# Optimization experiments

Measured on AMD Instinct MI355X. Metric: run time of the kernel, lower is better.

The kernel has to match this reference:

```python
import jax, jax.numpy as jnp
import numpy as np

B, IN_DIM, HID, ATT = 16384, 128, 512, 256
TOTAL = IN_DIM + HID + ATT


def setup_inputs() -> dict:
    key = jax.random.key(0)
    ks = jax.random.split(key, 10)
    u = lambda k, shape, lo, hi: jax.random.uniform(k, shape, jnp.float32, lo, hi)
    return {
        "t": jnp.float32(0.0),
        "h_ltc": jax.random.normal(ks[0], (B, HID), jnp.float32),
        "x_t": jax.random.normal(ks[1], (B, IN_DIM), jnp.float32),
        "context": jax.random.normal(ks[2], (B, ATT), jnp.float32),
        "W_gd": u(ks[3], (2 * HID, TOTAL), -0.1, 0.1),
        "b_gd": u(ks[4], (2 * HID,), -0.1, 0.1),
        "W_tau": u(ks[5], (HID, HID), -0.1, 0.1),
        "b_tau": u(ks[6], (HID,), -0.1, 0.1),
        "gleak": u(ks[7], (HID,), 0.001, 1.0),
        "cm": u(ks[8], (HID,), 0.4, 0.6),
    }


def reference(t, h_ltc, x_t, context, W_gd, b_gd, W_tau, b_tau, gleak, cm):
    # combined: [B, IN+HID+ATT]
    combined = jnp.concatenate([x_t, h_ltc, context], axis=1)
    g_d = combined @ W_gd.T + b_gd            # [B, 2*HID]
    gate, dynamics = jnp.split(g_d, 2, axis=1)
    tau = jax.nn.softplus(h_ltc @ W_tau.T + b_tau)  # [B, HID]
    numerator = jax.nn.sigmoid(gate) * jnp.tanh(dynamics) - h_ltc
    denominator = tau + jax.nn.softplus(cm) + jax.nn.softplus(gleak)
    return numerator / (denominator + 1e-6)
```

## Files before the change

### kernel.cpp

```cpp
#include <hip/hip_runtime.h>
#include <hip/hip_bf16.h>
#include <math.h>

#define BROWS 16384
#define IN_DIM 128
#define HID 512
#define ATT 256
#define KTOT 896
#define KC_TOT 112

typedef __bf16 bf16x8 __attribute__((ext_vector_type(8)));
typedef float f32x4 __attribute__((ext_vector_type(4)));

__device__ __forceinline__ float softplus_f(float x) {
    return fmaxf(x, 0.0f) + log1pf(__expf(-fabsf(x)));
}

__global__ void pack_B(const float* __restrict__ W_gd, const float* __restrict__ W_tau,
                       const float* __restrict__ gleak, const float* __restrict__ cm,
                       __hip_bfloat16* __restrict__ B_stage, float* __restrict__ dconst) {
    const int cid = blockIdx.x * 256 + threadIdx.x;
    if (cid < HID) {
        dconst[cid] = softplus_f(cm[cid]) + softplus_f(gleak[cid]) + 1e-6f;
    }
    const int nl = cid % 192;
    const int kc = (cid / 192) % KC_TOT;
    const int jt = cid / (192 * KC_TOT);
    const int jg = nl / 48, type = (nl % 48) / 16, j16 = nl % 16;
    const int j = jt * 64 + jg * 16 + j16;
    const int k0 = kc * 8;

    float v[8];
    if (type == 0) {
        const float* s = W_gd + (size_t)j * KTOT + k0;
        #pragma unroll
        for (int i = 0; i < 8; ++i) v[i] = s[i];
    } else if (type == 1) {
        const float* s = W_gd + (size_t)(HID + j) * KTOT + k0;
        #pragma unroll
        for (int i = 0; i < 8; ++i) v[i] = s[i];
    } else {
        if (k0 >= IN_DIM && k0 < IN_DIM + HID) {
            const float* s = W_tau + (size_t)j * HID + (k0 - IN_DIM);
            #pragma unroll
            for (int i = 0; i < 8; ++i) v[i] = s[i];
        } else {
            #pragma unroll
            for (int i = 0; i < 8; ++i) v[i] = 0.0f;
        }
    }
    union { __hip_bfloat16 hh[8]; uint4 u; } p;
    #pragma unroll
    for (int i = 0; i < 8; ++i) p.hh[i] = __float2bfloat16(v[i]);
    *(uint4*)(B_stage + (size_t)cid * 8) = p.u;
}

__global__ __launch_bounds__(512, 2) void ltc_gemm(
    const float* __restrict__ x, const float* __restrict__ h_ltc,
    const float* __restrict__ ctx, const __hip_bfloat16* __restrict__ B_stage,
    const float* __restrict__ b_gd, const float* __restrict__ b_tau,
    const float* __restrict__ dconst, float* __restrict__ out) {

    __shared__ __attribute__((aligned(16))) char As[57344];

    const int mt = blockIdx.x;
    const int tid = threadIdx.x;
    const int wave = tid >> 6, lane = tid & 63;
    const int q = lane >> 4, t = lane & 15;

    const int mi = tid >> 4;
    const int kcg = tid & 15;
    #pragma unroll
    for (int s = 0; s < 7; ++s) {
        const int kc = kcg + 16 * s;
        const float* src; int rs, col;
        if (s == 0)      { src = x;     rs = IN_DIM; col = kcg * 8; }
        else if (s < 5)  { src = h_ltc; rs = HID;    col = kcg * 8 + (s - 1) * 128; }
        else             { src = ctx;   rs = ATT;    col = kcg * 8 + (s - 5) * 128; }
        const float* p = src + (size_t)(mt * 32 + mi) * rs + col;
        float4 v0 = *(const float4*)p;
        float4 v1 = *(const float4*)(p + 4);
        union { __hip_bfloat16 hh[8]; uint4 u; } pk;
        pk.hh[0] = __float2bfloat16(v0.x); pk.hh[1] = __float2bfloat16(v0.y);
        pk.hh[2] = __float2bfloat16(v0.z); pk.hh[3] = __float2bfloat16(v0.w);
        pk.hh[4] = __float2bfloat16(v1.x); pk.hh[5] = __float2bfloat16(v1.y);
        pk.hh[6] = __float2bfloat16(v1.z); pk.hh[7] = __float2bfloat16(v1.w);
        *(uint4*)(As + ((kc * 32 + (mi ^ (kc & 31))) << 4)) = pk.u;
    }
    __syncthreads();

    for (int it = 0; it < 4; ++it) {
        const int jglob = it * 128 + wave * 16;
        const int jt = jglob >> 6;
        const int jg = (jglob >> 4) & 3;
        const __hip_bfloat16* bBase = B_stage
            + ((size_t)jt * (KC_TOT * 192) + jg * 48 + t) * 8;

        f32x4 acc[2][3];
        #pragma unroll
        for (int f = 0; f < 2; ++f)
            #pragma unroll
            for (int ty = 0; ty < 3; ++ty) acc[f][ty] = (f32x4)0.0f;

        bf16x8 ab[4][2]; bf16x8 bb[4][3];

        #pragma unroll
        for (int p = 0; p < 2; ++p) {
            const int kc = p * 4 + q;
            const int sw = kc & 31;
            ab[p][0] = *(const bf16x8*)(As + ((kc * 32 + (t ^ sw)) << 4));
            ab[p][1] = *(const bf16x8*)(As + ((kc * 32 + ((16 + t) ^ sw)) << 4));
        }
        #pragma unroll
        for (int p = 0; p < 3; ++p) {
            const __hip_bfloat16* bp = bBase + (size_t)(p * 4 + q) * 1536;
            bb[p][0] = *(const bf16x8*)(bp);
            bb[p][1] = *(const bf16x8*)(bp + 128);
        }

        #pragma unroll 4
        for (int kst = 0; kst < 28; ++kst) {
            const int ca = kst & 3;
            if (kst < 26) {
                const int kc = (kst + 2) * 4 + q;
                const int sw = kc & 31;
                const int na = (kst + 2) & 3;
                ab[na][0] = *(const bf16x8*)(As + ((kc * 32 + (t ^ sw)) << 4));
                ab[na][1] = *(const bf16x8*)(As + ((kc * 32 + ((16 + t) ^ sw)) << 4));
            }
            if (kst < 25) {
                const int kc = (kst + 3) * 4 + q;
                const int nbf = (kst + 3) & 3;
                const __hip_bfloat16* bp = bBase + (size_t)kc * 1536;
                bb[nbf][0] = *(const bf16x8*)(bp);
                bb[nbf][1] = *(const bf16x8*)(bp + 128);
                if (kst + 3 >= 4 && kst + 3 < 20)
                    bb[nbf][2] = *(const bf16x8*)(bp + 256);
            }
            const bool tau_cur = (kst >= 4 && kst < 20);
            acc[0][0] = __builtin_amdgcn_mfma_f32_16x16x32_bf16(ab[ca][0], bb[ca][0], acc[0][0], 0, 0, 0);
            acc[1][0] = __builtin_amdgcn_mfma_f32_16x16x32_bf16(ab[ca][1], bb[ca][0], acc[1][0], 0, 0, 0);
            acc[0][1] = __builtin_amdgcn_mfma_f32_16x16x32_bf16(ab[ca][0], bb[ca][1], acc[0][1], 0, 0, 0);
            acc[1][1] = __builtin_amdgcn_mfma_f32_16x16x32_bf16(ab[ca][1], bb[ca][1], acc[1][1], 0, 0, 0);
            if (tau_cur) {
                acc[0][2] = __builtin_amdgcn_mfma_f32_16x16x32_bf16(ab[ca][0], bb[ca][2], acc[0][2], 0, 0, 0);
                acc[1][2] = __builtin_amdgcn_mfma_f32_16x16x32_bf16(ab[ca][1], bb[ca][2], acc[1][2], 0, 0, 0);
            }
        }

        const int j = jglob + t;
        const float bgj = b_gd[j];
        const float bdj = b_gd[HID + j];
        const float btj = b_tau[j];
        const float dcj = dconst[j];
        #pragma unroll
        for (int f = 0; f < 2; ++f) {
            #pragma unroll
            for (int r = 0; r < 4; ++r) {
                const int row = mt * 32 + f * 16 + q * 4 + r;
                const float gv = acc[f][0][r] + bgj;
                const float dv = acc[f][1][r] + bdj;
                const float tp = acc[f][2][r] + btj;
                const float hv = h_ltc[(size_t)row * HID + j];
                const float sig = __builtin_amdgcn_rcpf(1.0f + __expf(-gv));
                const float th  = 1.0f - 2.0f * __builtin_amdgcn_rcpf(__expf(2.0f * dv) + 1.0f);
                const float tau = fmaxf(tp, 0.0f) + __logf(1.0f + __expf(-fabsf(tp)));
                out[(size_t)row * HID + j] = (sig * th - hv) * __builtin_amdgcn_rcpf(tau + dcj);
            }
        }
    }
}

extern "C" void kernel_launch(void* const* d_in, const int* in_sizes, int n_in,
                              void* d_out, int out_size, void* d_ws, size_t ws_size,
                              hipStream_t stream) {
    const float* h_ltc = (const float*)d_in[1];
    const float* x_t   = (const float*)d_in[2];
    const float* ctx   = (const float*)d_in[3];
    const float* W_gd  = (const float*)d_in[4];
    const float* b_gd  = (const float*)d_in[5];
    const float* W_tau = (const float*)d_in[6];
    const float* b_tau = (const float*)d_in[7];
    const float* gleak = (const float*)d_in[8];
    const float* cm    = (const float*)d_in[9];

    char* ws = (char*)d_ws;
    __hip_bfloat16* B_stage = (__hip_bfloat16*)ws;
    float* dconst = (float*)(ws + 2752512);

    pack_B<<<672, 256, 0, stream>>>(W_gd, W_tau, gleak, cm, B_stage, dconst);
    ltc_gemm<<<512, 512, 0, stream>>>(x_t, h_ltc, ctx, B_stage, b_gd, b_tau, dconst,
                                      (float*)d_out);
}
```

Baseline: 179.8 us.

## Restructure GEMM into 64x256 tiles with double-buffered LDS B staging

Each workgroup now computes a 64-row by 256-column output tile instead of 32 rows across all 512 columns. The weight tile is staged into LDS with asynchronous global-to-LDS loads and the activations are streamed per K-step, both double-buffered. Block indices are remapped so tiles sharing rows land on the same XCD. The aim is to replace per-wave global B reads with LDS reuse and to overlap loading with MFMA work, at the cost of a larger register accumulator set (24 f32x4) and a barrier every K-step.

```diff
diff --git a/kernel.cpp b/kernel.cpp
--- a/kernel.cpp
+++ b/kernel.cpp
@@ -55,112 +55,143 @@
     *(uint4*)(B_stage + (size_t)cid * 8) = p.u;
 }
 
+#define LDSB 49152
+#define LDSBUF 53248
+
 __global__ __launch_bounds__(512, 2) void ltc_gemm(
     const float* __restrict__ x, const float* __restrict__ h_ltc,
     const float* __restrict__ ctx, const __hip_bfloat16* __restrict__ B_stage,
     const float* __restrict__ b_gd, const float* __restrict__ b_tau,
     const float* __restrict__ dconst, float* __restrict__ out) {
 
-    __shared__ __attribute__((aligned(16))) char As[57344];
-
-    const int mt = blockIdx.x;
+    __shared__ __attribute__((aligned(16))) char Lds[2][LDSBUF];
+
+    const int wgid = blockIdx.x;
+    const int xcd = wgid & 7;
+    const int k2 = wgid >> 3;
+    const int jt2 = k2 & 1;
+    const int rt = xcd * 32 + (k2 >> 1);
+    const int jtBase = jt2 * 4;
+
     const int tid = threadIdx.x;
     const int wave = tid >> 6, lane = tid & 63;
     const int q = lane >> 4, t = lane & 15;
 
-    const int mi = tid >> 4;
-    const int kcg = tid & 15;
-    #pragma unroll
-    for (int s = 0; s < 7; ++s) {
-        const int kc = kcg + 16 * s;
-        const float* src; int rs, col;
-        if (s == 0)      { src = x;     rs = IN_DIM; col = kcg * 8; }
-        else if (s < 5)  { src = h_ltc; rs = HID;    col = kcg * 8 + (s - 1) * 128; }
-        else             { src = ctx;   rs = ATT;    col = kcg * 8 + (s - 5) * 128; }
-        const float* p = src + (size_t)(mt * 32 + mi) * rs + col;
+    int bo[6];
+    #pragma unroll
+    for (int i = 0; i < 6; ++i) {
+        const int n = i * 512 + tid;
+        const int kcl = n / 768;
+        const int jtl = (n / 192) & 3;
+        const int nl  = n - (n / 192) * 192;
+        bo[i] = (((jtBase + jtl) * KC_TOT + kcl) * 192 + nl) * 16;
+    }
+    const char* bsrc = (const char*)B_stage;
+
+    const int arow = (tid & 255) >> 2;
+    const int ach  = tid & 3;
+
+    #pragma unroll
+    for (int i = 0; i < 6; ++i) {
+        const int n = i * 512 + tid;
+        __builtin_amdgcn_global_load_lds(
+            (const __attribute__((address_space(1))) void*)(bsrc + bo[i]),
+            (__attribute__((address_space(3))) void*)(&Lds[0][n * 16]), 16, 0, 0);
+    }
+    if (tid < 256) {
+        const float* p = x + (size_t)(rt * 64 + arow) * IN_DIM + ach * 8;
         float4 v0 = *(const float4*)p;
         float4 v1 = *(const float4*)(p + 4);
         union { __hip_bfloat16 hh[8]; uint4 u; } pk;
-        pk.hh[0] = __float2bfloat16(v0.x); pk.hh[1] = __float2bfloat16(v0.y);
-        pk.hh[2] = __float2bfloat16(v0.z); pk.hh[3] = __float2bfloat16(v0.w);
-        pk.hh[4] = __float2bfloat16(v1.x); pk.hh[5] = __float2bfloat16(v1.y);
-        pk.hh[6] = __float2bfloat16(v1.z); pk.hh[7] = __float2bfloat16(v1.w);
-        *(uint4*)(As + ((kc * 32 + (mi ^ (kc & 31))) << 4)) = pk.u;
-    }
-    __syncthreads();
-
-    for (int it = 0; it < 4; ++it) {
-        const int jglob = it * 128 + wave * 16;
-        const int jt = jglob >> 6;
-        const int jg = (jglob >> 4) & 3;
-        const __hip_bfloat16* bBase = B_stage
-            + ((size_t)jt * (KC_TOT * 192) + jg * 48 + t) * 8;
-
-        f32x4 acc[2][3];
-        #pragma unroll
-        for (int f = 0; f < 2; ++f)
-            #pragma unroll
-            for (int ty = 0; ty < 3; ++ty) acc[f][ty] = (f32x4)0.0f;
-
-        bf16x8 ab[4][2]; bf16x8 bb[4][3];
-
-        #pragma unroll
-        for (int p = 0; p < 2; ++p) {
-            const int kc = p * 4 + q;
-            const int sw = kc & 31;
-            ab[p][0] = *(const bf16x8*)(As + ((kc * 32 + (t ^ sw)) << 4));
-            ab[p][1] = *(const bf16x8*)(As + ((kc * 32 + ((16 + t) ^ sw)) << 4));
-        }
-        #pragma unroll
-        for (int p = 0; p < 3; ++p) {
-            const __hip_bfloat16* bp = bBase + (size_t)(p * 4 + q) * 1536;
-            bb[p][0] = *(const bf16x8*)(bp);
-            bb[p][1] = *(const bf16x8*)(bp + 128);
-        }
-
-        #pragma unroll 4
-        for (int kst = 0; kst < 28; ++kst) {
-            const int ca = kst & 3;
-            if (kst < 26) {
-                const int kc = (kst + 2) * 4 + q;
-                const int sw = kc & 31;
-                const int na = (kst + 2) & 3;
-                ab[na][0] = *(const bf16x8*)(As + ((kc * 32 + (t ^ sw)) << 4));
-                ab[na][1] = *(const bf16x8*)(As + ((kc * 32 + ((16 + t) ^ sw)) << 4));
-            }
-            if (kst < 25) {
-                const int kc = (kst + 3) * 4 + q;
-                const int nbf = (kst + 3) & 3;
-                const __hip_bfloat16* bp = bBase + (size_t)kc * 1536;
-                bb[nbf][0] = *(const bf16x8*)(bp);
-                bb[nbf][1] = *(const bf16x8*)(bp + 128);
-                if (kst + 3 >= 4 && kst + 3 < 20)
-                    bb[nbf][2] = *(const bf16x8*)(bp + 256);
-            }
-            const bool tau_cur = (kst >= 4 && kst < 20);
-            acc[0][0] = __builtin_amdgcn_mfma_f32_16x16x32_bf16(ab[ca][0], bb[ca][0], acc[0][0], 0, 0, 0);
-            acc[1][0] = __builtin_amdgcn_mfma_f32_16x16x32_bf16(ab[ca][1], bb[ca][0], acc[1][0], 0, 0, 0);
-            acc[0][1] = __builtin_amdgcn_mfma_f32_16x16x32_bf16(ab[ca][0], bb[ca][1], acc[0][1], 0, 0, 0);
-            acc[1][1] = __builtin_amdgcn_mfma_f32_16x16x32_bf16(ab[ca][1], bb[ca][1], acc[1][1], 0, 0, 0);
-            if (tau_cur) {
-                acc[0][2] = __builtin_amdgcn_mfma_f32_16x16x32_bf16(ab[ca][0], bb[ca][2], acc[0][2], 0, 0, 0);
-                acc[1][2] = __builtin_amdgcn_mfma_f32_16x16x32_bf16(ab[ca][1], bb[ca][2], acc[1][2], 0, 0, 0);
-            }
-        }
-
-        const int j = jglob + t;
+        pk.hh[0]=__float2bfloat16(v0.x); pk.hh[1]=__float2bfloat16(v0.y);
+        pk.hh[2]=__float2bfloat16(v0.z); pk.hh[3]=__float2bfloat16(v0.w);
+        pk.hh[4]=__float2bfloat16(v1.x); pk.hh[5]=__float2bfloat16(v1.y);
+        pk.hh[6]=__float2bfloat16(v1.z); pk.hh[7]=__float2bfloat16(v1.w);
+        *(uint4*)(&Lds[0][LDSB + ((ach * 64 + (arow ^ (ach & 31))) << 4)]) = pk.u;
+    }
+
+    f32x4 acc[4][2][3];
+    #pragma unroll
+    for (int rf = 0; rf < 4; ++rf)
+        #pragma unroll
+        for (int jf = 0; jf < 2; ++jf)
+            #pragma unroll
+            for (int ty = 0; ty < 3; ++ty) acc[rf][jf][ty] = (f32x4)0.0f;
+
+    const int bOff = ((q * 4 + (wave >> 1)) * 192 + (wave & 1) * 96 + t) * 16;
+
+    for (int kw = 0; kw < 28; ++kw) {
+        const int cur = kw & 1, nxt = cur ^ 1;
+        __syncthreads();
+
+        float4 av0, av1;
+        const int kwn = kw + 1;
+        if (kw < 27) {
+            #pragma unroll
+            for (int i = 0; i < 6; ++i) {
+                bo[i] += 12288;
+                const int n = i * 512 + tid;
+                __builtin_amdgcn_global_load_lds(
+                    (const __attribute__((address_space(1))) void*)(bsrc + bo[i]),
+                    (__attribute__((address_space(3))) void*)(&Lds[nxt][n * 16]), 16, 0, 0);
+            }
+            if (tid < 256) {
+                const float* asrc; int ars, acol;
+                if (kwn < 4)       { asrc = x;     ars = IN_DIM; acol = kwn * 32; }
+                else if (kwn < 20) { asrc = h_ltc; ars = HID;    acol = kwn * 32 - 128; }
+                else               { asrc = ctx;   ars = ATT;    acol = kwn * 32 - 640; }
+                const float* p = asrc + (size_t)(rt * 64 + arow) * ars + acol + ach * 8;
+                av0 = *(const float4*)p;
+                av1 = *(const float4*)(p + 4);
+            }
+        }
+
+        const bool tau_cur = (kw >= 4 && kw < 20);
+        const char* Bc = Lds[cur];
+        const char* Ac = Lds[cur] + LDSB;
+        #pragma unroll
+        for (int jf = 0; jf < 2; ++jf) {
+            const bf16x8 bg = *(const bf16x8*)(Bc + bOff + jf * 768);
+            const bf16x8 bd = *(const bf16x8*)(Bc + bOff + jf * 768 + 256);
+            bf16x8 bt;
+            if (tau_cur) bt = *(const bf16x8*)(Bc + bOff + jf * 768 + 512);
+            #pragma unroll
+            for (int rf = 0; rf < 4; ++rf) {
+                const int row = rf * 16 + t;
+                const bf16x8 a = *(const bf16x8*)(Ac + ((q * 64 + (row ^ ((kw * 4 + q) & 31))) << 4));
+                acc[rf][jf][0] = __builtin_amdgcn_mfma_f32_16x16x32_bf16(a, bg, acc[rf][jf][0], 0, 0, 0);
+                acc[rf][jf][1] = __builtin_amdgcn_mfma_f32_16x16x32_bf16(a, bd, acc[rf][jf][1], 0, 0, 0);
+                if (tau_cur)
+                    acc[rf][jf][2] = __builtin_amdgcn_mfma_f32_16x16x32_bf16(a, bt, acc[rf][jf][2], 0, 0, 0);
+            }
+        }
+
+        if (kw < 27 && tid < 256) {
+            union { __hip_bfloat16 hh[8]; uint4 u; } pk;
+            pk.hh[0]=__float2bfloat16(av0.x); pk.hh[1]=__float2bfloat16(av0.y);
+            pk.hh[2]=__float2bfloat16(av0.z); pk.hh[3]=__float2bfloat16(av0.w);
+            pk.hh[4]=__float2bfloat16(av1.x); pk.hh[5]=__float2bfloat16(av1.y);
+            pk.hh[6]=__float2bfloat16(av1.z); pk.hh[7]=__float2bfloat16(av1.w);
+            *(uint4*)(&Lds[nxt][LDSB + ((ach * 64 + (arow ^ ((kwn * 4 + ach) & 31))) << 4)]) = pk.u;
+        }
+    }
+
+    const int j0 = jt2 * 256 + wave * 32;
+    #pragma unroll
+    for (int jf = 0; jf < 2; ++jf) {
+        const int j = j0 + jf * 16 + t;
         const float bgj = b_gd[j];
         const float bdj = b_gd[HID + j];
         const float btj = b_tau[j];
         const float dcj = dconst[j];
         #pragma unroll
-        for (int f = 0; f < 2; ++f) {
+        for (int rf = 0; rf < 4; ++rf) {
             #pragma unroll
             for (int r = 0; r < 4; ++r) {
-                const int row = mt * 32 + f * 16 + q * 4 + r;
-                const float gv = acc[f][0][r] + bgj;
-                const float dv = acc[f][1][r] + bdj;
-                const float tp = acc[f][2][r] + btj;
+                const int row = rt * 64 + rf * 16 + q * 4 + r;
+                const float gv = acc[rf][jf][0][r] + bgj;
+                const float dv = acc[rf][jf][1][r] + bdj;
+                const float tp = acc[rf][jf][2][r] + btj;
                 const float hv = h_ltc[(size_t)row * HID + j];
                 const float sig = __builtin_amdgcn_rcpf(1.0f + __expf(-gv));
                 const float th  = 1.0f - 2.0f * __builtin_amdgcn_rcpf(__expf(2.0f * dv) + 1.0f);
```

New measurement: 181.4 us. Within noise of the previous version (+0.9%).
